# Performance work log

Measured on AMD Instinct MI355X. Metric: run time of the kernel, lower is better.

The kernel has to match this reference:

```python
import jax, jax.numpy as jnp
import numpy as np

LENA, BATCH, ARR, HID = 8, 128, 1024, 64


def setup_inputs() -> dict:
    key = jax.random.key(0)
    ks = jax.random.split(key, 7)
    s = 0.1  # keep gates out of saturation
    return {
        "x": jax.random.normal(ks[0], (BATCH, ARR, 1), jnp.float32),
        "hn": jnp.zeros((LENA, BATCH, HID), jnp.float32),  # per-LSTM h0 (torch (1,B,H) squeezed)
        "Wih": jax.random.normal(ks[1], (LENA, 4 * HID, 1), jnp.float32) * s,
        "Whh": jax.random.normal(ks[2], (LENA, 4 * HID, HID), jnp.float32) * s,
        "bih": jax.random.normal(ks[3], (LENA, 4 * HID), jnp.float32) * s,
        "bhh": jax.random.normal(ks[4], (LENA, 4 * HID), jnp.float32) * s,
        "Wl": jax.random.normal(ks[5], (LENA, ARR), jnp.float32) * s,
        "bl": jax.random.normal(ks[6], (LENA,), jnp.float32) * s,
    }


def _ensemble_lstm_last_unit(x, hn, Wih, Whh, bias):
    # x: (B, T); hn: (L, B, H). All L LSTMs run fused in one scan over time.
    L, B, H = hn.shape
    c0 = jnp.zeros_like(hn)

    def step(carry, x_t):  # x_t: (B,)
        h, c = carry  # (L, B, H)
        gates = (x_t[None, :, None] * Wih[:, None, :, 0]
                 + jnp.einsum('lbh,lgh->lbg', h, Whh)
                 + bias[:, None, :])  # (L, B, 4H)
        i, f, g, o = jnp.split(gates, 4, axis=-1)  # torch gate order i,f,g,o
        i, f, o = jax.nn.sigmoid(i), jax.nn.sigmoid(f), jax.nn.sigmoid(o)
        c = f * c + i * jnp.tanh(g)
        h = o * jnp.tanh(c)
        return (h, c), h[:, :, -1]  # emit last hidden unit: o[:, :, -1]

    _, ys = jax.lax.scan(step, (hn, c0), x.T)  # ys: (T, L, B)
    return ys


def reference(x, hn, Wih, Whh, bih, bhh, Wl, bl):
    bias = bih + bhh  # (L, 4H)
    ys = _ensemble_lstm_last_unit(x[:, :, 0], hn, Wih, Whh, bias)  # (T, L, B)
    r = ys.sum(axis=1).T  # sum over ensemble -> (B, T=arr_size)
    return r @ Wl.T + bl  # (B, lenA)
```

## Files before the change

kernel.cpp:

```cpp
#include <hip/hip_runtime.h>


#define LENA 8
#define NB 128
#define NT 1024
#define NH 64

typedef __attribute__((ext_vector_type(4))) float f32x4;
typedef __attribute__((ext_vector_type(8))) short bf16x8;

__device__ __forceinline__ short f2bf(float f) {
    unsigned u = __float_as_uint(f);
    unsigned r = (u + 0x7FFFu + ((u >> 16) & 1u)) >> 16;
    return (short)r;
}

__global__ __launch_bounds__(256, 2) void lstm_v13_kernel(
    const float* __restrict__ x, const float* __restrict__ hn,
    const float* __restrict__ Wih, const float* __restrict__ Whh,
    const float* __restrict__ bih, const float* __restrict__ bhh,
    const float* __restrict__ Wl, float* __restrict__ ws)
{
    __shared__ float x2[NT][2];
    __shared__ float ring[NT][2];
    __shared__ __align__(16) short hbuf[2][16][8];
    __shared__ float pws[2][2][8];

    const int tid = threadIdx.x;
    const int w   = tid >> 6;
    const int l   = tid & 63;
    const int col = l & 15;
    const int kg  = l >> 4;
    const int bb  = kg & 1;
    const int li  = blockIdx.x >> 6;
    const int bg  = blockIdx.x & 63;
    const int b0  = bg * 2;

    for (int i = tid; i < 2 * NT; i += 256) {
        int bx = i >> 10, t = i & (NT - 1);
        x2[t][bx] = x[(size_t)(b0 + bx) * NT + t];
    }
    if (tid < 128) {
        int b = tid >> 6, u = tid & 63;
        float v = hn[((size_t)li * NB + b0 + b) * NH + u];
        int slot = b * 8 + ((u >> 3) ^ (2 * b));
        hbuf[0][slot][u & 7] = f2bf(v);
    }

    const float RLN2 = 1.44269504f;
    bf16x8 bf[4][2];
    #pragma unroll
    for (int g = 0; g < 4; ++g) {
        const float sc = (g == 2) ? 2.0f * RLN2 : RLN2;
        const float* rp = Whh + ((size_t)li * 256 + 64 * g + 16 * w + col) * 64 + kg * 8;
        #pragma unroll
        for (int kh = 0; kh < 2; ++kh) {
            const float* q = rp + kh * 32;
            bf16x8 f;
            #pragma unroll
            for (int e = 0; e < 8; ++e) f[e] = f2bf(sc * q[e]);
            bf[g][kh] = f;
        }
    }
    const int u_c = 16 * w + col;
    float wih4[4];
    f32x4 cinit[4];
    #pragma unroll
    for (int g = 0; g < 4; ++g) {
        const float sc = (g == 2) ? 2.0f * RLN2 : RLN2;
        int rowc = li * 256 + 64 * g + u_c;
        wih4[g] = sc * Wih[rowc];
        float bv = sc * (bih[rowc] + bhh[rowc]);
        cinit[g][0] = bv; cinit[g][1] = bv; cinit[g][2] = bv; cinit[g][3] = bv;
    }

    const int b_r = col & 1;
    const int s0 = b_r * 8 + (kg ^ (2 * b_r));
    const int s1 = b_r * 8 + ((4 + kg) ^ (2 * b_r));
    const int wslot = bb * 8 + ((u_c >> 3) ^ (2 * bb));
    const int wpos  = u_c & 7;
    const bool isring = (u_c == 63);

    float cst = 0.0f;

    __syncthreads();

    #pragma unroll 2
    for (int t = 0; t < NT; ++t) {
        const int p = t & 1;
        bf16x8 a0 = *(const bf16x8*)&hbuf[p][s0][0];
        bf16x8 a1 = *(const bf16x8*)&hbuf[p][s1][0];
        const float xv = x2[t][bb];

        f32x4 acc[4];
        __builtin_amdgcn_s_setprio(1);
        #pragma unroll
        for (int g = 0; g < 4; ++g) {
            f32x4 a = __builtin_amdgcn_mfma_f32_16x16x32_bf16(a0, bf[g][0], cinit[g], 0, 0, 0);
            acc[g] = __builtin_amdgcn_mfma_f32_16x16x32_bf16(a1, bf[g][1], a, 0, 0, 0);
        }
        __builtin_amdgcn_s_setprio(0);
        __builtin_amdgcn_sched_barrier(0);

        float gi = fmaf(xv, wih4[0], bb ? acc[0][1] : acc[0][0]);
        float gf = fmaf(xv, wih4[1], bb ? acc[1][1] : acc[1][0]);
        float gg = fmaf(xv, wih4[2], bb ? acc[2][1] : acc[2][0]);
        float go = fmaf(xv, wih4[3], bb ? acc[3][1] : acc[3][0]);

        float iv = __builtin_amdgcn_rcpf(1.0f + __builtin_amdgcn_exp2f(-gi));
        float fv = __builtin_amdgcn_rcpf(1.0f + __builtin_amdgcn_exp2f(-gf));
        float gt = fmaf(-5.77078016f, __builtin_amdgcn_rcpf(1.0f + __builtin_amdgcn_exp2f(gg)), 2.88539008f);
        float ov = __builtin_amdgcn_rcpf(1.0f + __builtin_amdgcn_exp2f(-go));
        cst = fmaf(fv, cst, iv * gt);
        float ct = fmaf(-2.0f, __builtin_amdgcn_rcpf(1.0f + __builtin_amdgcn_exp2f(cst)), 1.0f);
        float hh = ov * ct;

        unsigned pk;
        asm("v_cvt_pk_bf16_f32 %0, %1, %2" : "=v"(pk) : "v"(hh), "v"(hh));
        hbuf[p ^ 1][wslot][wpos] = (short)(pk & 0xffffu);
        if (isring) ring[t][bb] = hh;
        __syncthreads();
    }

    {
        const int b = w >> 1, p2 = w & 1;
        const int a = l & 7, ch = l >> 3;
        const int tb = p2 * 512 + ch * 64;
        const float* wlp = Wl + (size_t)a * NT + tb;
        float pacc = 0.0f;
        #pragma unroll 4
        for (int i = 0; i < 64; ++i)
            pacc = fmaf(ring[tb + i][b], wlp[i], pacc);
        pacc += __shfl_xor(pacc, 8);
        pacc += __shfl_xor(pacc, 16);
        pacc += __shfl_xor(pacc, 32);
        if (l < 8) pws[b][p2][a] = pacc;
    }
    __syncthreads();
    if (tid < 16) {
        int b = tid >> 3, a = tid & 7;
        ws[((size_t)blockIdx.x * 2 + b) * 8 + a] = pws[b][0][a] + pws[b][1][a];
    }
}

__global__ __launch_bounds__(256) void reduce_kernel(
    const float* __restrict__ ws, const float* __restrict__ bl, float* __restrict__ out)
{
    int tid = blockIdx.x * 256 + threadIdx.x;
    if (tid >= NB * LENA) return;
    int b = tid >> 3, a = tid & 7;
    int bg = b >> 1, bx = b & 1;
    float s = bl[a];
    #pragma unroll
    for (int li = 0; li < LENA; ++li)
        s += ws[(((size_t)li * 64 + bg) * 2 + bx) * 8 + a];
    out[tid] = s;
}

extern "C" void kernel_launch(void* const* d_in, const int* in_sizes, int n_in,
                              void* d_out, int out_size, void* d_ws, size_t ws_size,
                              hipStream_t stream) {
    const float* x   = (const float*)d_in[0];
    const float* hn  = (const float*)d_in[1];
    const float* Wih = (const float*)d_in[2];
    const float* Whh = (const float*)d_in[3];
    const float* bih = (const float*)d_in[4];
    const float* bhh = (const float*)d_in[5];
    const float* Wl  = (const float*)d_in[6];
    const float* bl  = (const float*)d_in[7];
    float* out = (float*)d_out;
    float* ws  = (float*)d_ws;

    lstm_v13_kernel<<<dim3(512), dim3(256), 0, stream>>>(x, hn, Wih, Whh, bih, bhh, Wl, ws);
    reduce_kernel<<<dim3(4), dim3(256), 0, stream>>>(ws, bl, out);
}
```

Baseline: 255.0 us.

## Split LSTM recurrence K-dimension across two wave groups with 4 batches per block

Each block now handles 4 batch rows instead of 2 and uses 8 waves. The K=64 hidden reduction is split across two wave halves, so each wave issues one MFMA per gate instead of two chained ones. Partial sums from the upper half go through shared memory, and only the lower half computes the activations. This shortens the serial MFMA chain per timestep and halves the block count, at the cost of an extra __syncthreads and an LDS round-trip on every step.

```diff
diff --git a/kernel.cpp b/kernel.cpp
--- a/kernel.cpp
+++ b/kernel.cpp
@@ -15,32 +15,34 @@
     return (short)r;
 }
 
-__global__ __launch_bounds__(256, 2) void lstm_v13_kernel(
+__global__ __launch_bounds__(512, 2) void lstm_v14_kernel(
     const float* __restrict__ x, const float* __restrict__ hn,
     const float* __restrict__ Wih, const float* __restrict__ Whh,
     const float* __restrict__ bih, const float* __restrict__ bhh,
     const float* __restrict__ Wl, float* __restrict__ ws)
 {
-    __shared__ float x2[NT][2];
-    __shared__ float ring[NT][2];
-    __shared__ __align__(16) short hbuf[2][16][8];
-    __shared__ float pws[2][2][8];
+    __shared__ float x4[NT][4];
+    __shared__ float ring[NT][4];
+    __shared__ __align__(16) short hbuf[2][32][8];
+    __shared__ __align__(16) float pbuf[4][4][16][4];
+    __shared__ float pws[8][8];
 
     const int tid = threadIdx.x;
     const int w   = tid >> 6;
+    const int pw  = w & 3;
+    const int kh  = w >> 2;
     const int l   = tid & 63;
     const int col = l & 15;
     const int kg  = l >> 4;
-    const int bb  = kg & 1;
-    const int li  = blockIdx.x >> 6;
-    const int bg  = blockIdx.x & 63;
-    const int b0  = bg * 2;
+    const int li  = blockIdx.x >> 5;
+    const int bg  = blockIdx.x & 31;
+    const int b0  = bg * 4;
 
-    for (int i = tid; i < 2 * NT; i += 256) {
+    for (int i = tid; i < 4 * NT; i += 512) {
         int bx = i >> 10, t = i & (NT - 1);
-        x2[t][bx] = x[(size_t)(b0 + bx) * NT + t];
+        x4[t][bx] = x[(size_t)(b0 + bx) * NT + t];
     }
-    if (tid < 128) {
+    if (tid < 256) {
         int b = tid >> 6, u = tid & 63;
         float v = hn[((size_t)li * NB + b0 + b) * NH + u];
         int slot = b * 8 + ((u >> 3) ^ (2 * b));
@@ -48,21 +50,17 @@
     }
 
     const float RLN2 = 1.44269504f;
-    bf16x8 bf[4][2];
+    bf16x8 bfr[4];
     #pragma unroll
     for (int g = 0; g < 4; ++g) {
         const float sc = (g == 2) ? 2.0f * RLN2 : RLN2;
-        const float* rp = Whh + ((size_t)li * 256 + 64 * g + 16 * w + col) * 64 + kg * 8;
+        const float* q = Whh + ((size_t)li * 256 + 64 * g + 16 * pw + col) * 64 + kh * 32 + kg * 8;
+        bf16x8 f;
         #pragma unroll
-        for (int kh = 0; kh < 2; ++kh) {
-            const float* q = rp + kh * 32;
-            bf16x8 f;
-            #pragma unroll
-            for (int e = 0; e < 8; ++e) f[e] = f2bf(sc * q[e]);
-            bf[g][kh] = f;
-        }
+        for (int e = 0; e < 8; ++e) f[e] = f2bf(sc * q[e]);
+        bfr[g] = f;
     }
-    const int u_c = 16 * w + col;
+    const int u_c = 16 * pw + col;
     float wih4[4];
     f32x4 cinit[4];
     #pragma unroll
@@ -70,14 +68,13 @@
         const float sc = (g == 2) ? 2.0f * RLN2 : RLN2;
         int rowc = li * 256 + 64 * g + u_c;
         wih4[g] = sc * Wih[rowc];
-        float bv = sc * (bih[rowc] + bhh[rowc]);
+        float bv = (kh == 0) ? sc * (bih[rowc] + bhh[rowc]) : 0.0f;
         cinit[g][0] = bv; cinit[g][1] = bv; cinit[g][2] = bv; cinit[g][3] = bv;
     }
 
-    const int b_r = col & 1;
-    const int s0 = b_r * 8 + (kg ^ (2 * b_r));
-    const int s1 = b_r * 8 + ((4 + kg) ^ (2 * b_r));
-    const int wslot = bb * 8 + ((u_c >> 3) ^ (2 * bb));
+    const int b_r = col & 3;
+    const int sA = b_r * 8 + (((kh << 2) + kg) ^ (2 * b_r));
+    const int wslot = kg * 8 + ((u_c >> 3) ^ (2 * kg));
     const int wpos  = u_c & 7;
     const bool isring = (u_c == 63);
 
@@ -88,44 +85,57 @@
     #pragma unroll 2
     for (int t = 0; t < NT; ++t) {
         const int p = t & 1;
-        bf16x8 a0 = *(const bf16x8*)&hbuf[p][s0][0];
-        bf16x8 a1 = *(const bf16x8*)&hbuf[p][s1][0];
-        const float xv = x2[t][bb];
+        bf16x8 a = *(const bf16x8*)&hbuf[p][sA][0];
 
         f32x4 acc[4];
         __builtin_amdgcn_s_setprio(1);
         #pragma unroll
-        for (int g = 0; g < 4; ++g) {
-            f32x4 a = __builtin_amdgcn_mfma_f32_16x16x32_bf16(a0, bf[g][0], cinit[g], 0, 0, 0);
-            acc[g] = __builtin_amdgcn_mfma_f32_16x16x32_bf16(a1, bf[g][1], a, 0, 0, 0);
-        }
+        for (int g = 0; g < 4; ++g)
+            acc[g] = __builtin_amdgcn_mfma_f32_16x16x32_bf16(a, bfr[g], cinit[g], 0, 0, 0);
         __builtin_amdgcn_s_setprio(0);
         __builtin_amdgcn_sched_barrier(0);
 
-        float gi = fmaf(xv, wih4[0], bb ? acc[0][1] : acc[0][0]);
-        float gf = fmaf(xv, wih4[1], bb ? acc[1][1] : acc[1][0]);
-        float gg = fmaf(xv, wih4[2], bb ? acc[2][1] : acc[2][0]);
-        float go = fmaf(xv, wih4[3], bb ? acc[3][1] : acc[3][0]);
+        f32x4 se;
+        #pragma unroll
+        for (int g = 0; g < 4; ++g) {
+            float va = (kg & 1) ? acc[g][1] : acc[g][0];
+            float vb = (kg & 1) ? acc[g][3] : acc[g][2];
+            se[g] = (kg & 2) ? vb : va;
+        }
 
-        float iv = __builtin_amdgcn_rcpf(1.0f + __builtin_amdgcn_exp2f(-gi));
-        float fv = __builtin_amdgcn_rcpf(1.0f + __builtin_amdgcn_exp2f(-gf));
-        float gt = fmaf(-5.77078016f, __builtin_amdgcn_rcpf(1.0f + __builtin_amdgcn_exp2f(gg)), 2.88539008f);
-        float ov = __builtin_amdgcn_rcpf(1.0f + __builtin_amdgcn_exp2f(-go));
-        cst = fmaf(fv, cst, iv * gt);
-        float ct = fmaf(-2.0f, __builtin_amdgcn_rcpf(1.0f + __builtin_amdgcn_exp2f(cst)), 1.0f);
-        float hh = ov * ct;
+        if (kh) {
+            *(f32x4*)&pbuf[pw][kg][col][0] = se;
+        }
+        __syncthreads();
 
-        unsigned pk;
-        asm("v_cvt_pk_bf16_f32 %0, %1, %2" : "=v"(pk) : "v"(hh), "v"(hh));
-        hbuf[p ^ 1][wslot][wpos] = (short)(pk & 0xffffu);
-        if (isring) ring[t][bb] = hh;
+        if (!kh) {
+            f32x4 pp = *(const f32x4*)&pbuf[pw][kg][col][0];
+            const float xv = x4[t][kg];
+            float gi = fmaf(xv, wih4[0], se[0] + pp[0]);
+            float gf = fmaf(xv, wih4[1], se[1] + pp[1]);
+            float gg = fmaf(xv, wih4[2], se[2] + pp[2]);
+            float go = fmaf(xv, wih4[3], se[3] + pp[3]);
+
+            float iv = __builtin_amdgcn_rcpf(1.0f + __builtin_amdgcn_exp2f(-gi));
+            float fv = __builtin_amdgcn_rcpf(1.0f + __builtin_amdgcn_exp2f(-gf));
+            float gt = fmaf(-5.77078016f, __builtin_amdgcn_rcpf(1.0f + __builtin_amdgcn_exp2f(gg)), 2.88539008f);
+            float ov = __builtin_amdgcn_rcpf(1.0f + __builtin_amdgcn_exp2f(-go));
+            cst = fmaf(fv, cst, iv * gt);
+            float ct = fmaf(-2.0f, __builtin_amdgcn_rcpf(1.0f + __builtin_amdgcn_exp2f(cst)), 1.0f);
+            float hh = ov * ct;
+
+            unsigned pk;
+            asm("v_cvt_pk_bf16_f32 %0, %1, %2" : "=v"(pk) : "v"(hh), "v"(hh));
+            hbuf[p ^ 1][wslot][wpos] = (short)(pk & 0xffffu);
+            if (isring) ring[t][kg] = hh;
+        }
         __syncthreads();
     }
 
     {
-        const int b = w >> 1, p2 = w & 1;
+        const int b = w & 3, hf = w >> 2;
         const int a = l & 7, ch = l >> 3;
-        const int tb = p2 * 512 + ch * 64;
+        const int tb = hf * 512 + ch * 64;
         const float* wlp = Wl + (size_t)a * NT + tb;
         float pacc = 0.0f;
         #pragma unroll 4
@@ -134,12 +144,12 @@
         pacc += __shfl_xor(pacc, 8);
         pacc += __shfl_xor(pacc, 16);
         pacc += __shfl_xor(pacc, 32);
-        if (l < 8) pws[b][p2][a] = pacc;
+        if (l < 8) pws[w][a] = pacc;
     }
     __syncthreads();
-    if (tid < 16) {
+    if (tid < 32) {
         int b = tid >> 3, a = tid & 7;
-        ws[((size_t)blockIdx.x * 2 + b) * 8 + a] = pws[b][0][a] + pws[b][1][a];
+        ws[(size_t)blockIdx.x * 32 + b * 8 + a] = pws[b][a] + pws[b + 4][a];
     }
 }
 
@@ -149,11 +159,11 @@
     int tid = blockIdx.x * 256 + threadIdx.x;
     if (tid >= NB * LENA) return;
     int b = tid >> 3, a = tid & 7;
-    int bg = b >> 1, bx = b & 1;
+    int bg = b >> 2, bx = b & 3;
     float s = bl[a];
     #pragma unroll
     for (int li = 0; li < LENA; ++li)
-        s += ws[(((size_t)li * 64 + bg) * 2 + bx) * 8 + a];
+        s += ws[((size_t)(li * 32 + bg)) * 32 + bx * 8 + a];
     out[tid] = s;
 }
 
@@ -171,6 +181,6 @@
     float* out = (float*)d_out;
     float* ws  = (float*)d_ws;
 
-    lstm_v13_kernel<<<dim3(512), dim3(256), 0, stream>>>(x, hn, Wih, Whh, bih, bhh, Wl, ws);
+    lstm_v14_kernel<<<dim3(256), dim3(512), 0, stream>>>(x, hn, Wih, Whh, bih, bhh, Wl, ws);
     reduce_kernel<<<dim3(4), dim3(256), 0, stream>>>(ws, bl, out);
 }
```

Result: slower. 401.0 us (+57.3%).
